# Performance work log

Hardware: AMD Instinct MI355X
Metric: run time of the kernel (lower is better)

Reference implementation:

```python
import jax, jax.numpy as jnp
import numpy as np

EMBED_DIM = 1024
NUM_HEADS = 16
HEAD_DIM = EMBED_DIM // NUM_HEADS


def setup_inputs() -> dict:
    key = jax.random.key(0)
    ks = jax.random.split(key, 5)
    B, S, D = 2, 2048, EMBED_DIM
    scale = 1.0 / np.sqrt(D)
    x = jax.random.normal(ks[0], (B, S, D), dtype=jnp.float32)
    W_qkv = jax.random.normal(ks[1], (D, 3 * D), dtype=jnp.float32) * scale
    b_qkv = jnp.zeros((3 * D,), dtype=jnp.float32)
    W_out = jax.random.normal(ks[2], (D, D), dtype=jnp.float32) * scale
    b_out = jnp.zeros((D,), dtype=jnp.float32)
    return {"x": x, "W_qkv": W_qkv, "b_qkv": b_qkv, "W_out": W_out, "b_out": b_out}


def reference(x, W_qkv, b_qkv, W_out, b_out):
    B, S, D = x.shape
    H, Hd = NUM_HEADS, HEAD_DIM
    qkv = x @ W_qkv + b_qkv                       # [B,S,3D]
    qkv = qkv.reshape(B, S, 3, H, Hd)
    q = qkv[:, :, 0].transpose(0, 2, 1, 3)        # [B,H,S,Hd]
    k = qkv[:, :, 1].transpose(0, 2, 1, 3)
    v = qkv[:, :, 2].transpose(0, 2, 1, 3)
    scores = jnp.einsum('bhqd,bhkd->bhqk', q, k) / np.sqrt(Hd)  # [B,H,S,S]
    causal = jnp.tril(jnp.ones((S, S), dtype=bool))
    scores = jnp.where(causal[None, None], scores, -jnp.inf)
    attn = jax.nn.softmax(scores, axis=-1)
    out = jnp.einsum('bhqk,bhkd->bhqd', attn, v)  # [B,H,S,Hd]
    out = out.transpose(0, 2, 1, 3).reshape(B, S, D)
    return out @ W_out + b_out
```

## Files before the change

kernel.cpp:

```cpp
#include <hip/hip_runtime.h>
#include <hip/hip_bf16.h>
#include <math.h>

#define EMBED_DIM 1024
#define NUM_HEADS 16
#define HEAD_DIM 64
#define BATCH 2
#define SEQ 2048

using short8  = __attribute__((ext_vector_type(8))) short;
using floatx4 = __attribute__((ext_vector_type(4))) float;

__device__ __forceinline__ ushort f2bf(float f) {
    unsigned u = __float_as_uint(f);
    u = (u + 0x7FFFu + ((u >> 16) & 1u)) >> 16;
    return (ushort)u;
}

__device__ __forceinline__ unsigned bfpack2(float a, float b) {
    return ((__float_as_uint(a) + 0x8000u) >> 16) |
           (((__float_as_uint(b) + 0x8000u) >> 16) << 16);
}

__device__ __forceinline__ void load_lds16(const ushort* g, ushort* l) {
    __builtin_amdgcn_global_load_lds(
        (const __attribute__((address_space(1))) void*)g,
        (__attribute__((address_space(3))) void*)l, 16, 0, 0);
}

__device__ __forceinline__ void tc_tile(
    const float* __restrict__ W, ushort* __restrict__ Wt,
    int K, int N, int n0, int k0, float (*t)[65])
{
    const int c = threadIdx.x & 63, r0 = (threadIdx.x >> 6) * 16;
    #pragma unroll
    for (int r = 0; r < 16; ++r)
        t[r0 + r][c] = W[(size_t)(k0 + r0 + r) * N + n0 + c];
    __syncthreads();
    #pragma unroll
    for (int r = 0; r < 16; ++r)
        Wt[(size_t)(n0 + r0 + r) * K + k0 + c] = f2bf(t[c][r0 + r]);
}

__global__ __launch_bounds__(256) void prep_all(
    const float* __restrict__ x, const float* __restrict__ W_qkv,
    const float* __restrict__ W_out,
    ushort* __restrict__ xb, ushort* __restrict__ Wqb_t, ushort* __restrict__ Wob_t)
{
    __shared__ float t[64][65];
    const int bx = blockIdx.x;
    if (bx < 4096) {
        int i = (bx * 256 + threadIdx.x) * 4;
        float4 v = *(const float4*)&x[i];
        ushort4 o = { f2bf(v.x), f2bf(v.y), f2bf(v.z), f2bf(v.w) };
        *(ushort4*)&xb[i] = o;
    } else if (bx < 4096 + 768) {
        int b = bx - 4096;
        tc_tile(W_qkv, Wqb_t, 1024, 3072, (b % 48) * 64, (b / 48) * 64, t);
    } else {
        int b = bx - 4864;
        tc_tile(W_out, Wob_t, 1024, 1024, (b % 16) * 64, (b / 16) * 64, t);
    }
}

#define GK 1024

__device__ __forceinline__ void gemm_core(
    const ushort* __restrict__ A, const ushort* __restrict__ Bt,
    int m0, int n0, ushort* As0, ushort* As1, ushort* Bs0, ushort* Bs1,
    floatx4 acc[4][4])
{
    const int tid  = threadIdx.x;
    const int w    = tid >> 6;
    const int lane = tid & 63;
    const int col  = lane & 15;
    const int quad = lane >> 4;
    const int wm   = w >> 1, wn = w & 1;

    #pragma unroll
    for (int i = 0; i < 4; ++i)
        #pragma unroll
        for (int j = 0; j < 4; ++j)
            acc[i][j] = (floatx4){0.f, 0.f, 0.f, 0.f};

    const int o0   = w * 2048 + lane * 16;
    const int row0 = o0 >> 6;
    const int ke0  = (o0 & 63) >> 1;
    const int loff = (w * 2048) >> 1;

    const ushort* ga = A  + (size_t)(m0 + row0) * GK + ke0;
    const ushort* gb = Bt + (size_t)(n0 + row0) * GK + ke0;

    #pragma unroll
    for (int t = 0; t < 2; ++t) {
        load_lds16(ga + (size_t)t * 16 * GK, As0 + loff + t * 512);
        load_lds16(gb + (size_t)t * 16 * GK, Bs0 + loff + t * 512);
    }
    __syncthreads();

    for (int k0 = 0; k0 < GK; k0 += 32) {
        const int cur = (k0 >> 5) & 1;
        ushort* Ac = cur ? As1 : As0;
        ushort* Bc = cur ? Bs1 : Bs0;
        ushort* An = cur ? As0 : As1;
        ushort* Bn = cur ? Bs0 : Bs1;

        if (k0 + 32 < GK) {
            #pragma unroll
            for (int t = 0; t < 2; ++t) {
                load_lds16(ga + (k0 + 32) + (size_t)t * 16 * GK, An + loff + t * 512);
                load_lds16(gb + (k0 + 32) + (size_t)t * 16 * GK, Bn + loff + t * 512);
            }
        }

        short8 af[4], bf[4];
        #pragma unroll
        for (int i = 0; i < 4; ++i)
            af[i] = *(const short8*)&Ac[(wm * 64 + i * 16 + col) * 32 + quad * 8];
        #pragma unroll
        for (int j = 0; j < 4; ++j)
            bf[j] = *(const short8*)&Bc[(wn * 64 + j * 16 + col) * 32 + quad * 8];
        #pragma unroll
        for (int i = 0; i < 4; ++i)
            #pragma unroll
            for (int j = 0; j < 4; ++j)
                acc[i][j] = __builtin_amdgcn_mfma_f32_16x16x32_bf16(af[i], bf[j], acc[i][j], 0, 0, 0);

        __syncthreads();
    }
}

__device__ __forceinline__ void gemm_core64(
    const ushort* __restrict__ A, const ushort* __restrict__ Bt,
    int m0, int n0, ushort* As0, ushort* As1, ushort* Bs0, ushort* Bs1,
    floatx4 acc[4][2])
{
    const int tid  = threadIdx.x;
    const int w    = tid >> 6;
    const int lane = tid & 63;
    const int col  = lane & 15;
    const int quad = lane >> 4;
    const int wm   = w >> 1, wn = w & 1;

    #pragma unroll
    for (int i = 0; i < 4; ++i)
        #pragma unroll
        for (int j = 0; j < 2; ++j)
            acc[i][j] = (floatx4){0.f, 0.f, 0.f, 0.f};

    const int row0 = w * 16 + (lane >> 2);
    const int ke0  = ((lane & 3) ^ ((lane >> 3) & 3)) * 8;
    const int loff = w * 512;

    const ushort* ga = A  + (size_t)(m0 + row0) * GK + ke0;
    const ushort* gb = Bt + (size_t)(n0 + row0) * GK + ke0;

    load_lds16(ga,               As0 + loff);
    load_lds16(ga + 64 * GK,     As0 + loff + 2048);
    load_lds16(gb,               Bs0 + loff);
    __syncthreads();

    const int sq = (quad ^ ((col >> 1) & 3)) * 8;

    for (int k0 = 0; k0 < GK; k0 += 32) {
        const int cur = (k0 >> 5) & 1;
        ushort* Ac = cur ? As1 : As0;
        ushort* Bc = cur ? Bs1 : Bs0;
        ushort* An = cur ? As0 : As1;
        ushort* Bn = cur ? Bs0 : Bs1;

        if (k0 + 32 < GK) {
            load_lds16(ga + (k0 + 32),           An + loff);
            load_lds16(ga + (k0 + 32) + 64 * GK, An + loff + 2048);
            load_lds16(gb + (k0 + 32),           Bn + loff);
        }

        short8 af[4], bf[2];
        #pragma unroll
        for (int i = 0; i < 4; ++i)
            af[i] = *(const short8*)&Ac[(wm * 64 + i * 16 + col) * 32 + sq];
        #pragma unroll
        for (int j = 0; j < 2; ++j)
            bf[j] = *(const short8*)&Bc[(wn * 32 + j * 16 + col) * 32 + sq];
        #pragma unroll
        for (int i = 0; i < 4; ++i)
            #pragma unroll
            for (int j = 0; j < 2; ++j)
                acc[i][j] = __builtin_amdgcn_mfma_f32_16x16x32_bf16(af[i], bf[j], acc[i][j], 0, 0, 0);

        __syncthreads();
    }
}

__global__ __launch_bounds__(256) void gemm_qkv_mfma(
    const ushort* __restrict__ A, const ushort* __restrict__ Bt,
    const float* __restrict__ bias,
    ushort* __restrict__ Qb, ushort* __restrict__ Kb, ushort* __restrict__ Vt)
{
    __shared__ __align__(16) ushort As[2][128 * 32];
    __shared__ __align__(16) ushort Bs[2][128 * 32];
    const int n0 = blockIdx.x * 128;
    const int m0 = blockIdx.y * 128;

    floatx4 acc[4][4];
    gemm_core(A, Bt, m0, n0, As[0], As[1], Bs[0], Bs[1], acc);

    const int lane = threadIdx.x & 63;
    const int w    = threadIdx.x >> 6;
    const int col  = lane & 15, quad = lane >> 4;
    const int wm   = w >> 1, wn = w & 1;

    #pragma unroll
    for (int j = 0; j < 4; ++j) {
        const int n = n0 + wn * 64 + j * 16 + col;
        const float bj = bias[n];
        const int part = n >> 10;
        const int h = (n >> 6) & 15;
        const int d = n & 63;
        #pragma unroll
        for (int i = 0; i < 4; ++i)
            #pragma unroll
            for (int r = 0; r < 4; ++r) {
                const int m = m0 + wm * 64 + i * 16 + quad * 4 + r;
                const int b = m >> 11, s = m & 2047;
                const int bh = b * 16 + h;
                const ushort bv = f2bf(acc[i][j][r] + bj);
                if (part == 0)      Qb[((size_t)bh * SEQ + s) * 64 + d] = bv;
                else if (part == 1) Kb[((size_t)bh * SEQ + s) * 64 + d] = bv;
                else                Vt[((size_t)bh * 64 + d) * SEQ + s] = bv;
            }
    }
}

__global__ __launch_bounds__(256) void gemm_out_mfma(
    const ushort* __restrict__ A, const ushort* __restrict__ Bt,
    const float* __restrict__ bias, float* __restrict__ out)
{
    __shared__ __align__(16) ushort As[2][128 * 32];
    __shared__ __align__(16) ushort Bs[2][64 * 32];
    const int n0 = blockIdx.x * 64;
    const int m0 = blockIdx.y * 128;

    floatx4 acc[4][2];
    gemm_core64(A, Bt, m0, n0, As[0], As[1], Bs[0], Bs[1], acc);

    const int lane = threadIdx.x & 63;
    const int w    = threadIdx.x >> 6;
    const int col  = lane & 15, quad = lane >> 4;
    const int wm   = w >> 1, wn = w & 1;

    #pragma unroll
    for (int j = 0; j < 2; ++j) {
        const int n = n0 + wn * 32 + j * 16 + col;
        const float bj = bias[n];
        #pragma unroll
        for (int i = 0; i < 4; ++i)
            #pragma unroll
            for (int r = 0; r < 4; ++r) {
                const int m = m0 + wm * 64 + i * 16 + quad * 4 + r;
                out[(size_t)m * EMBED_DIM + n] = acc[i][j][r] + bj;
            }
    }
}

#define LP 72

__global__ __launch_bounds__(256) void attn_fused(
    const ushort* __restrict__ Qb, const ushort* __restrict__ Kb,
    const ushort* __restrict__ Vt, ushort* __restrict__ out)
{
    const int id = blockIdx.x;
    const int qt = 31 - (id >> 5);
    const int bh = id & 31;
    const int b  = bh >> 4, h = bh & 15;
    const int q0 = qt * 64;

    __shared__ __align__(16) ushort Qs[8 * 512];
    __shared__ __align__(16) ushort Ks[2][8 * 512];
    __shared__ __align__(16) ushort Vs[2][8 * 512];
    __shared__ __align__(16) ushort Ps[64 * LP];
    __shared__ __align__(16) float  ls[4][16];

    const int tid  = threadIdx.x;
    const int w    = tid >> 6;
    const int lane = tid & 63;
    const int col  = lane & 15;
    const int quad = lane >> 4;

    const ushort* kg[2];
    const ushort* vg[2];
    #pragma unroll
    for (int t = 0; t < 2; ++t) {
        kg[t] = Kb + (size_t)bh * SEQ * 64 + (size_t)(w * 16 + col) * 64 + t * 32 + quad * 8;
        vg[t] = Vt + (size_t)bh * 64 * SEQ + (size_t)(w * 16 + col) * SEQ + t * 32 + quad * 8;
    }

    {
        const ushort* Qg = Qb + ((size_t)bh * SEQ + q0) * 64;
        #pragma unroll
        for (int t = 0; t < 2; ++t) {
            load_lds16(Qg + (size_t)(w * 16 + col) * 64 + t * 32 + quad * 8,
                       &Qs[(w * 2 + t) * 512]);
            load_lds16(kg[t], &Ks[0][(w * 2 + t) * 512]);
            load_lds16(vg[t], &Vs[0][(w * 2 + t) * 512]);
            kg[t] += 64 * 64;
            vg[t] += 64;
        }
    }
    __syncthreads();

    const short8 a0 = *(const short8*)&Qs[(w * 2 + 0) * 512 + lane * 8];
    const short8 a1 = *(const short8*)&Qs[(w * 2 + 1) * 512 + lane * 8];

    floatx4 acc_o[4];
    #pragma unroll
    for (int dbi = 0; dbi < 4; ++dbi) acc_o[dbi] = (floatx4){0.f, 0.f, 0.f, 0.f};
    float l_lane = 0.f;
    const int myq = w * 16 + col;

    for (int kt = 0; kt <= qt; ++kt) {
        const int cur = kt & 1;
        const ushort* Kc = Ks[cur];
        const ushort* Vc = Vs[cur];

        if (kt < qt) {
            ushort* Kn = (ushort*)Ks[cur ^ 1];
            ushort* Vn = (ushort*)Vs[cur ^ 1];
            #pragma unroll
            for (int t = 0; t < 2; ++t) {
                load_lds16(kg[t], &Kn[(w * 2 + t) * 512]);
                load_lds16(vg[t], &Vn[(w * 2 + t) * 512]);
                kg[t] += 64 * 64;
                vg[t] += 64;
            }
        }

        floatx4 s_acc[4];
        #pragma unroll
        for (int kb = 0; kb < 4; ++kb) {
            short8 k0f = *(const short8*)&Kc[(kb * 2 + 0) * 512 + lane * 8];
            short8 k1f = *(const short8*)&Kc[(kb * 2 + 1) * 512 + lane * 8];
            floatx4 z = (floatx4){0.f, 0.f, 0.f, 0.f};
            z = __builtin_amdgcn_mfma_f32_16x16x32_bf16(k0f, a0, z, 0, 0, 0);
            z = __builtin_amdgcn_mfma_f32_16x16x32_bf16(k1f, a1, z, 0, 0, 0);
            s_acc[kb] = z;
        }

        if (kt == qt) {
            #pragma unroll
            for (int kb = 0; kb < 4; ++kb) {
                const int kbase = kb * 16 + quad * 4;
                float p[4];
                #pragma unroll
                for (int r = 0; r < 4; ++r) {
                    float e = __expf(s_acc[kb][r] * 0.125f);
                    p[r] = (kbase + r > myq) ? 0.f : e;
                    l_lane += p[r];
                }
                uint2 u = { bfpack2(p[0], p[1]), bfpack2(p[2], p[3]) };
                *(uint2*)&Ps[myq * LP + kbase] = u;
            }
        } else {
            #pragma unroll
            for (int kb = 0; kb < 4; ++kb) {
                const int kbase = kb * 16 + quad * 4;
                float p[4];
                #pragma unroll
                for (int r = 0; r < 4; ++r) {
                    p[r] = __expf(s_acc[kb][r] * 0.125f);
                    l_lane += p[r];
                }
                uint2 u = { bfpack2(p[0], p[1]), bfpack2(p[2], p[3]) };
                *(uint2*)&Ps[myq * LP + kbase] = u;
            }
        }

        short8 pa0 = *(const short8*)&Ps[(w * 16 + col) * LP + quad * 8];
        short8 pa1 = *(const short8*)&Ps[(w * 16 + col) * LP + 32 + quad * 8];
        #pragma unroll
        for (int dbi = 0; dbi < 4; ++dbi) {
            short8 vb0 = *(const short8*)&Vc[(dbi * 2 + 0) * 512 + lane * 8];
            short8 vb1 = *(const short8*)&Vc[(dbi * 2 + 1) * 512 + lane * 8];
            acc_o[dbi] = __builtin_amdgcn_mfma_f32_16x16x32_bf16(pa0, vb0, acc_o[dbi], 0, 0, 0);
            acc_o[dbi] = __builtin_amdgcn_mfma_f32_16x16x32_bf16(pa1, vb1, acc_o[dbi], 0, 0, 0);
        }

        __syncthreads();
    }

    l_lane += __shfl_xor(l_lane, 16);
    l_lane += __shfl_xor(l_lane, 32);
    if (quad == 0) ls[w][col] = 1.f / l_lane;
    float4 invv = *(const float4*)&ls[w][quad * 4];

    #pragma unroll
    for (int dbi = 0; dbi < 4; ++dbi)
        #pragma unroll
        for (int r = 0; r < 4; ++r) {
            int q = q0 + w * 16 + quad * 4 + r;
            int d = dbi * 16 + col;
            float inv = (r == 0) ? invv.x : (r == 1) ? invv.y : (r == 2) ? invv.z : invv.w;
            out[((size_t)(b * SEQ + q)) * EMBED_DIM + h * 64 + d] = f2bf(acc_o[dbi][r] * inv);
        }
}

extern "C" void kernel_launch(void* const* d_in, const int* in_sizes, int n_in,
                              void* d_out, int out_size, void* d_ws, size_t ws_size,
                              hipStream_t stream)
{
    const float* x     = (const float*)d_in[0];
    const float* W_qkv = (const float*)d_in[1];
    const float* b_qkv = (const float*)d_in[2];
    const float* W_out = (const float*)d_in[3];
    const float* b_out = (const float*)d_in[4];
    float* out = (float*)d_out;

    const int M  = BATCH * SEQ;
    const int D  = EMBED_DIM;
    const int N1 = 3 * D;
    const size_t HE = (size_t)BATCH * NUM_HEADS * SEQ * 64;

    ushort* xb    = (ushort*)d_ws;
    ushort* Wqb_t = xb + (size_t)M * D;
    ushort* Wob_t = Wqb_t + (size_t)D * N1;
    ushort* Qb    = Wob_t + (size_t)D * D;
    ushort* Kb    = Qb + HE;
    ushort* Vt    = Kb + HE;
    ushort* attnb = Vt + HE;

    prep_all<<<5120, 256, 0, stream>>>(x, W_qkv, W_out, xb, Wqb_t, Wob_t);

    gemm_qkv_mfma<<<dim3(N1 / 128, M / 128), 256, 0, stream>>>(
        xb, Wqb_t, b_qkv, Qb, Kb, Vt);

    attn_fused<<<dim3(32 * 32), 256, 0, stream>>>(Qb, Kb, Vt, attnb);

    gemm_out_mfma<<<dim3(D / 64, M / 128), 256, 0, stream>>>(
        attnb, Wob_t, b_out, out);
}
```

Before: 188.8 us.

## Load Q/K/V fragments directly from global into registers, dropping LDS staging

The attention kernel no longer stages Q, K and V tiles through double-buffered shared memory. Each wave now reads its MFMA operand fragments straight from global memory (relying on L1/L2 for reuse across the four waves), and the per-iteration block barrier is removed. This cuts LDS traffic, shared-memory footprint and synchronisation. In exchange, each wave issues redundant global loads for K and V with no software prefetch, so load latency may be exposed. Ps is still written and read per wave without a barrier, which is safe only because each wave touches its own rows.

Measured after the change: 276.6 us. 1.47x slower.

```diff
diff --git a/kernel.cpp b/kernel.cpp
--- a/kernel.cpp
+++ b/kernel.cpp
@@ -275,9 +275,6 @@
     const int b  = bh >> 4, h = bh & 15;
     const int q0 = qt * 64;
 
-    __shared__ __align__(16) ushort Qs[8 * 512];
-    __shared__ __align__(16) ushort Ks[2][8 * 512];
-    __shared__ __align__(16) ushort Vs[2][8 * 512];
     __shared__ __align__(16) ushort Ps[64 * LP];
     __shared__ __align__(16) float  ls[4][16];
 
@@ -287,30 +284,12 @@
     const int col  = lane & 15;
     const int quad = lane >> 4;
 
-    const ushort* kg[2];
-    const ushort* vg[2];
-    #pragma unroll
-    for (int t = 0; t < 2; ++t) {
-        kg[t] = Kb + (size_t)bh * SEQ * 64 + (size_t)(w * 16 + col) * 64 + t * 32 + quad * 8;
-        vg[t] = Vt + (size_t)bh * 64 * SEQ + (size_t)(w * 16 + col) * SEQ + t * 32 + quad * 8;
-    }
-
-    {
-        const ushort* Qg = Qb + ((size_t)bh * SEQ + q0) * 64;
-        #pragma unroll
-        for (int t = 0; t < 2; ++t) {
-            load_lds16(Qg + (size_t)(w * 16 + col) * 64 + t * 32 + quad * 8,
-                       &Qs[(w * 2 + t) * 512]);
-            load_lds16(kg[t], &Ks[0][(w * 2 + t) * 512]);
-            load_lds16(vg[t], &Vs[0][(w * 2 + t) * 512]);
-            kg[t] += 64 * 64;
-            vg[t] += 64;
-        }
-    }
-    __syncthreads();
-
-    const short8 a0 = *(const short8*)&Qs[(w * 2 + 0) * 512 + lane * 8];
-    const short8 a1 = *(const short8*)&Qs[(w * 2 + 1) * 512 + lane * 8];
+    const ushort* Qg = Qb + ((size_t)bh * SEQ + q0 + w * 16 + col) * 64 + quad * 8;
+    const short8 a0 = *(const short8*)&Qg[0];
+    const short8 a1 = *(const short8*)&Qg[32];
+
+    const ushort* Kg = Kb + (size_t)bh * SEQ * 64 + (size_t)col * 64 + quad * 8;
+    const ushort* Vg = Vt + ((size_t)bh * 64 + col) * SEQ + quad * 8;
 
     floatx4 acc_o[4];
     #pragma unroll
@@ -319,30 +298,28 @@
     const int myq = w * 16 + col;
 
     for (int kt = 0; kt <= qt; ++kt) {
-        const int cur = kt & 1;
-        const ushort* Kc = Ks[cur];
-        const ushort* Vc = Vs[cur];
-
-        if (kt < qt) {
-            ushort* Kn = (ushort*)Ks[cur ^ 1];
-            ushort* Vn = (ushort*)Vs[cur ^ 1];
-            #pragma unroll
-            for (int t = 0; t < 2; ++t) {
-                load_lds16(kg[t], &Kn[(w * 2 + t) * 512]);
-                load_lds16(vg[t], &Vn[(w * 2 + t) * 512]);
-                kg[t] += 64 * 64;
-                vg[t] += 64;
-            }
+        const ushort* Kt_ = Kg + (size_t)kt * 64 * 64;
+        const ushort* Vt_ = Vg + kt * 64;
+
+        short8 kf[4][2];
+        #pragma unroll
+        for (int kb = 0; kb < 4; ++kb) {
+            kf[kb][0] = *(const short8*)&Kt_[(size_t)(kb * 16) * 64];
+            kf[kb][1] = *(const short8*)&Kt_[(size_t)(kb * 16) * 64 + 32];
+        }
+        short8 vb[4][2];
+        #pragma unroll
+        for (int dbi = 0; dbi < 4; ++dbi) {
+            vb[dbi][0] = *(const short8*)&Vt_[(size_t)dbi * 16 * SEQ];
+            vb[dbi][1] = *(const short8*)&Vt_[(size_t)dbi * 16 * SEQ + 32];
         }
 
         floatx4 s_acc[4];
         #pragma unroll
         for (int kb = 0; kb < 4; ++kb) {
-            short8 k0f = *(const short8*)&Kc[(kb * 2 + 0) * 512 + lane * 8];
-            short8 k1f = *(const short8*)&Kc[(kb * 2 + 1) * 512 + lane * 8];
             floatx4 z = (floatx4){0.f, 0.f, 0.f, 0.f};
-            z = __builtin_amdgcn_mfma_f32_16x16x32_bf16(k0f, a0, z, 0, 0, 0);
-            z = __builtin_amdgcn_mfma_f32_16x16x32_bf16(k1f, a1, z, 0, 0, 0);
+            z = __builtin_amdgcn_mfma_f32_16x16x32_bf16(kf[kb][0], a0, z, 0, 0, 0);
+            z = __builtin_amdgcn_mfma_f32_16x16x32_bf16(kf[kb][1], a1, z, 0, 0, 0);
             s_acc[kb] = z;
         }
 
@@ -379,13 +356,9 @@
         short8 pa1 = *(const short8*)&Ps[(w * 16 + col) * LP + 32 + quad * 8];
         #pragma unroll
         for (int dbi = 0; dbi < 4; ++dbi) {
-            short8 vb0 = *(const short8*)&Vc[(dbi * 2 + 0) * 512 + lane * 8];
-            short8 vb1 = *(const short8*)&Vc[(dbi * 2 + 1) * 512 + lane * 8];
-            acc_o[dbi] = __builtin_amdgcn_mfma_f32_16x16x32_bf16(pa0, vb0, acc_o[dbi], 0, 0, 0);
-            acc_o[dbi] = __builtin_amdgcn_mfma_f32_16x16x32_bf16(pa1, vb1, acc_o[dbi], 0, 0, 0);
-        }
-
-        __syncthreads();
+            acc_o[dbi] = __builtin_amdgcn_mfma_f32_16x16x32_bf16(pa0, vb[dbi][0], acc_o[dbi], 0, 0, 0);
+            acc_o[dbi] = __builtin_amdgcn_mfma_f32_16x16x32_bf16(pa1, vb[dbi][1], acc_o[dbi], 0, 0, 0);
+        }
     }
 
     l_lane += __shfl_xor(l_lane, 16);
```

## Pair causal query tiles per block to share K/V loads and balance work

Applied to the files above, without the earlier changes.

Each attention block now handles two query tiles, j and 31-j, for the same batch-head. They share one pass over the K/V tiles: K and V fragments are loaded once from LDS into registers and fed to both tiles' MFMAs. This gives every block the same amount of causal work (33 tile-steps) and halves the grid to 512 blocks. Q is read straight from global memory into registers instead of staging through LDS. In exchange, register pressure rises from the double accumulators and the cached K/V fragments, which may lower occupancy.

Result: slower. 197.0 us (+4.3%).

```diff
diff --git a/kernel.cpp b/kernel.cpp
--- a/kernel.cpp
+++ b/kernel.cpp
@@ -270,16 +270,16 @@
     const ushort* __restrict__ Vt, ushort* __restrict__ out)
 {
     const int id = blockIdx.x;
-    const int qt = 31 - (id >> 5);
+    const int j  = id >> 5;
     const int bh = id & 31;
     const int b  = bh >> 4, h = bh & 15;
-    const int q0 = qt * 64;
-
-    __shared__ __align__(16) ushort Qs[8 * 512];
+    const int qtA = j, qtB = 31 - j;
+    const int q0A = qtA * 64, q0B = qtB * 64;
+
     __shared__ __align__(16) ushort Ks[2][8 * 512];
     __shared__ __align__(16) ushort Vs[2][8 * 512];
     __shared__ __align__(16) ushort Ps[64 * LP];
-    __shared__ __align__(16) float  ls[4][16];
+    __shared__ __align__(16) float  lsA[4][16], lsB[4][16];
 
     const int tid  = threadIdx.x;
     const int w    = tid >> 6;
@@ -295,35 +295,37 @@
         vg[t] = Vt + (size_t)bh * 64 * SEQ + (size_t)(w * 16 + col) * SEQ + t * 32 + quad * 8;
     }
 
-    {
-        const ushort* Qg = Qb + ((size_t)bh * SEQ + q0) * 64;
-        #pragma unroll
-        for (int t = 0; t < 2; ++t) {
-            load_lds16(Qg + (size_t)(w * 16 + col) * 64 + t * 32 + quad * 8,
-                       &Qs[(w * 2 + t) * 512]);
-            load_lds16(kg[t], &Ks[0][(w * 2 + t) * 512]);
-            load_lds16(vg[t], &Vs[0][(w * 2 + t) * 512]);
-            kg[t] += 64 * 64;
-            vg[t] += 64;
-        }
+    const ushort* QgA = Qb + ((size_t)bh * SEQ + q0A + w * 16 + col) * 64 + quad * 8;
+    const ushort* QgB = Qb + ((size_t)bh * SEQ + q0B + w * 16 + col) * 64 + quad * 8;
+    const short8 aA0 = *(const short8*)&QgA[0];
+    const short8 aA1 = *(const short8*)&QgA[32];
+    const short8 aB0 = *(const short8*)&QgB[0];
+    const short8 aB1 = *(const short8*)&QgB[32];
+
+    #pragma unroll
+    for (int t = 0; t < 2; ++t) {
+        load_lds16(kg[t], &Ks[0][(w * 2 + t) * 512]);
+        load_lds16(vg[t], &Vs[0][(w * 2 + t) * 512]);
+        kg[t] += 64 * 64;
+        vg[t] += 64;
     }
     __syncthreads();
 
-    const short8 a0 = *(const short8*)&Qs[(w * 2 + 0) * 512 + lane * 8];
-    const short8 a1 = *(const short8*)&Qs[(w * 2 + 1) * 512 + lane * 8];
-
-    floatx4 acc_o[4];
-    #pragma unroll
-    for (int dbi = 0; dbi < 4; ++dbi) acc_o[dbi] = (floatx4){0.f, 0.f, 0.f, 0.f};
-    float l_lane = 0.f;
+    floatx4 accA[4], accB[4];
+    #pragma unroll
+    for (int dbi = 0; dbi < 4; ++dbi) {
+        accA[dbi] = (floatx4){0.f, 0.f, 0.f, 0.f};
+        accB[dbi] = (floatx4){0.f, 0.f, 0.f, 0.f};
+    }
+    float lA = 0.f, lB = 0.f;
     const int myq = w * 16 + col;
 
-    for (int kt = 0; kt <= qt; ++kt) {
+    for (int kt = 0; kt <= qtB; ++kt) {
         const int cur = kt & 1;
         const ushort* Kc = Ks[cur];
         const ushort* Vc = Vs[cur];
 
-        if (kt < qt) {
+        if (kt < qtB) {
             ushort* Kn = (ushort*)Ks[cur ^ 1];
             ushort* Vn = (ushort*)Vs[cur ^ 1];
             #pragma unroll
@@ -335,18 +337,28 @@
             }
         }
 
-        floatx4 s_acc[4];
+        short8 kf[4][2], vf[4][2];
         #pragma unroll
         for (int kb = 0; kb < 4; ++kb) {
-            short8 k0f = *(const short8*)&Kc[(kb * 2 + 0) * 512 + lane * 8];
-            short8 k1f = *(const short8*)&Kc[(kb * 2 + 1) * 512 + lane * 8];
-            floatx4 z = (floatx4){0.f, 0.f, 0.f, 0.f};
-            z = __builtin_amdgcn_mfma_f32_16x16x32_bf16(k0f, a0, z, 0, 0, 0);
-            z = __builtin_amdgcn_mfma_f32_16x16x32_bf16(k1f, a1, z, 0, 0, 0);
-            s_acc[kb] = z;
-        }
-
-        if (kt == qt) {
+            kf[kb][0] = *(const short8*)&Kc[(kb * 2 + 0) * 512 + lane * 8];
+            kf[kb][1] = *(const short8*)&Kc[(kb * 2 + 1) * 512 + lane * 8];
+        }
+        #pragma unroll
+        for (int dbi = 0; dbi < 4; ++dbi) {
+            vf[dbi][0] = *(const short8*)&Vc[(dbi * 2 + 0) * 512 + lane * 8];
+            vf[dbi][1] = *(const short8*)&Vc[(dbi * 2 + 1) * 512 + lane * 8];
+        }
+
+        if (kt <= qtA) {
+            floatx4 s_acc[4];
+            #pragma unroll
+            for (int kb = 0; kb < 4; ++kb) {
+                floatx4 z = (floatx4){0.f, 0.f, 0.f, 0.f};
+                z = __builtin_amdgcn_mfma_f32_16x16x32_bf16(kf[kb][0], aA0, z, 0, 0, 0);
+                z = __builtin_amdgcn_mfma_f32_16x16x32_bf16(kf[kb][1], aA1, z, 0, 0, 0);
+                s_acc[kb] = z;
+            }
+            const bool diag = (kt == qtA);
             #pragma unroll
             for (int kb = 0; kb < 4; ++kb) {
                 const int kbase = kb * 16 + quad * 4;
@@ -354,53 +366,73 @@
                 #pragma unroll
                 for (int r = 0; r < 4; ++r) {
                     float e = __expf(s_acc[kb][r] * 0.125f);
-                    p[r] = (kbase + r > myq) ? 0.f : e;
-                    l_lane += p[r];
+                    p[r] = (diag && (kbase + r > myq)) ? 0.f : e;
+                    lA += p[r];
                 }
                 uint2 u = { bfpack2(p[0], p[1]), bfpack2(p[2], p[3]) };
                 *(uint2*)&Ps[myq * LP + kbase] = u;
             }
-        } else {
+            short8 pa0 = *(const short8*)&Ps[myq * LP + quad * 8];
+            short8 pa1 = *(const short8*)&Ps[myq * LP + 32 + quad * 8];
+            #pragma unroll
+            for (int dbi = 0; dbi < 4; ++dbi) {
+                accA[dbi] = __builtin_amdgcn_mfma_f32_16x16x32_bf16(pa0, vf[dbi][0], accA[dbi], 0, 0, 0);
+                accA[dbi] = __builtin_amdgcn_mfma_f32_16x16x32_bf16(pa1, vf[dbi][1], accA[dbi], 0, 0, 0);
+            }
+        }
+
+        {
+            floatx4 s_acc[4];
+            #pragma unroll
+            for (int kb = 0; kb < 4; ++kb) {
+                floatx4 z = (floatx4){0.f, 0.f, 0.f, 0.f};
+                z = __builtin_amdgcn_mfma_f32_16x16x32_bf16(kf[kb][0], aB0, z, 0, 0, 0);
+                z = __builtin_amdgcn_mfma_f32_16x16x32_bf16(kf[kb][1], aB1, z, 0, 0, 0);
+                s_acc[kb] = z;
+            }
+            const bool diag = (kt == qtB);
             #pragma unroll
             for (int kb = 0; kb < 4; ++kb) {
                 const int kbase = kb * 16 + quad * 4;
                 float p[4];
                 #pragma unroll
                 for (int r = 0; r < 4; ++r) {
-                    p[r] = __expf(s_acc[kb][r] * 0.125f);
-                    l_lane += p[r];
+                    float e = __expf(s_acc[kb][r] * 0.125f);
+                    p[r] = (diag && (kbase + r > myq)) ? 0.f : e;
+                    lB += p[r];
                 }
                 uint2 u = { bfpack2(p[0], p[1]), bfpack2(p[2], p[3]) };
                 *(uint2*)&Ps[myq * LP + kbase] = u;
             }
-        }
-
-        short8 pa0 = *(const short8*)&Ps[(w * 16 + col) * LP + quad * 8];
-        short8 pa1 = *(const short8*)&Ps[(w * 16 + col) * LP + 32 + quad * 8];
-        #pragma unroll
-        for (int dbi = 0; dbi < 4; ++dbi) {
-            short8 vb0 = *(const short8*)&Vc[(dbi * 2 + 0) * 512 + lane * 8];
-            short8 vb1 = *(const short8*)&Vc[(dbi * 2 + 1) * 512 + lane * 8];
-            acc_o[dbi] = __builtin_amdgcn_mfma_f32_16x16x32_bf16(pa0, vb0, acc_o[dbi], 0, 0, 0);
-            acc_o[dbi] = __builtin_amdgcn_mfma_f32_16x16x32_bf16(pa1, vb1, acc_o[dbi], 0, 0, 0);
+            short8 pa0 = *(const short8*)&Ps[myq * LP + quad * 8];
+            short8 pa1 = *(const short8*)&Ps[myq * LP + 32 + quad * 8];
+            #pragma unroll
+            for (int dbi = 0; dbi < 4; ++dbi) {
+                accB[dbi] = __builtin_amdgcn_mfma_f32_16x16x32_bf16(pa0, vf[dbi][0], accB[dbi], 0, 0, 0);
+                accB[dbi] = __builtin_amdgcn_mfma_f32_16x16x32_bf16(pa1, vf[dbi][1], accB[dbi], 0, 0, 0);
+            }
         }
 
         __syncthreads();
     }
 
-    l_lane += __shfl_xor(l_lane, 16);
-    l_lane += __shfl_xor(l_lane, 32);
-    if (quad == 0) ls[w][col] = 1.f / l_lane;
-    float4 invv = *(const float4*)&ls[w][quad * 4];
+    lA += __shfl_xor(lA, 16); lA += __shfl_xor(lA, 32);
+    lB += __shfl_xor(lB, 16); lB += __shfl_xor(lB, 32);
+    if (quad == 0) { lsA[w][col] = 1.f / lA; lsB[w][col] = 1.f / lB; }
+    float4 invA = *(const float4*)&lsA[w][quad * 4];
+    float4 invB = *(const float4*)&lsB[w][quad * 4];
 
     #pragma unroll
     for (int dbi = 0; dbi < 4; ++dbi)
         #pragma unroll
         for (int r = 0; r < 4; ++r) {
-            int q = q0 + w * 16 + quad * 4 + r;
-            int d = dbi * 16 + col;
-            float inv = (r == 0) ? invv.x : (r == 1) ? invv.y : (r == 2) ? invv.z : invv.w;
-            out[((size_t)(b * SEQ + q)) * EMBED_DIM + h * 64 + d] = f2bf(acc_o[dbi][r] * inv);
+            const int d = dbi * 16 + col;
+            const int qa = q0A + w * 16 + quad * 4 + r;
+            const int qb_ = q0B + w * 16 + quad * 4 + r;
+            const float ia = (r == 0) ? invA.x : (r == 1) ? invA.y : (r == 2) ? invA.z : invA.w;
+            const float ib = (r == 0) ? invB.x : (r == 1) ? invB.y : (r == 2) ? invB.z : invB.w;
+            out[((size_t)(b * SEQ + qa)) * EMBED_DIM + h * 64 + d] = f2bf(accA[dbi][r] * ia);
+            out[((size_t)(b * SEQ + qb_)) * EMBED_DIM + h * 64 + d] = f2bf(accB[dbi][r] * ib);
         }
 }
 
@@ -433,7 +465,7 @@
     gemm_qkv_mfma<<<dim3(N1 / 128, M / 128), 256, 0, stream>>>(
         xb, Wqb_t, b_qkv, Qb, Kb, Vt);
 
-    attn_fused<<<dim3(32 * 32), 256, 0, stream>>>(Qb, Kb, Vt, attnb);
+    attn_fused<<<dim3(512), 256, 0, stream>>>(Qb, Kb, Vt, attnb);
 
     gemm_out_mfma<<<dim3(D / 64, M / 128), 256, 0, stream>>>(
         attnb, Wob_t, b_out, out);
```
